# Performance work log

Measured on AMD Instinct MI355X. Metric: run time of the kernel, lower is better.

The kernel has to match this reference:

```python
import jax, jax.numpy as jnp
import numpy as np

D_MODEL = 4096
D_FF = 14336
T = 8192


def setup_inputs() -> dict:
    key = jax.random.key(0)
    k1, k2, k3, k4, k5 = jax.random.split(key, 5)
    s_in = 1.0 / np.sqrt(D_MODEL)
    s_ff = 1.0 / np.sqrt(D_FF)
    return {
        "hidden_states": jax.random.normal(k1, (T, D_MODEL), dtype=jnp.float32),
        "routing_weights": jax.random.uniform(k2, (T, 1), dtype=jnp.float32),
        "w_gate": jax.random.normal(k3, (D_MODEL, D_FF), dtype=jnp.float32) * s_in,
        "w_up": jax.random.normal(k4, (D_MODEL, D_FF), dtype=jnp.float32) * s_in,
        "w_down": jax.random.normal(k5, (D_FF, D_MODEL), dtype=jnp.float32) * s_ff,
    }


def reference(hidden_states, routing_weights, w_gate, w_up, w_down):
    # SwiGLU expert MLP: down(silu(gate(x)) * up(x)), scaled by routing weight
    gate = jnp.einsum("td,df->tf", hidden_states, w_gate)  # [T, D_FF]
    up = jnp.einsum("td,df->tf", hidden_states, w_up)      # [T, D_FF]
    h = jax.nn.silu(gate) * up                               # fused SwiGLU
    out = jnp.einsum("tf,fd->td", h, w_down)                 # [T, D_MODEL]
    return routing_weights * out
```

## Files before the change

kernel.cpp:

```cpp
#include <hip/hip_runtime.h>
#include <hip/hip_bf16.h>

using bf16 = __hip_bfloat16;
typedef __attribute__((ext_vector_type(8))) short bf16x8;
typedef __attribute__((ext_vector_type(4))) float f32x4;
typedef __attribute__((ext_vector_type(4))) int i32x4;

#define T_DIM 8192
#define DM    4096
#define DFF   14336

#define MFMA(va, vb, vc) __builtin_amdgcn_mfma_f32_16x16x32_bf16(va, vb, vc, 0, 0, 0)

__device__ __forceinline__ void gld_lds16(const bf16* gsrc, bf16* ldst) {
  auto* g = (const __attribute__((address_space(1))) unsigned int*)gsrc;
  auto* l = (__attribute__((address_space(3))) unsigned int*)ldst;
  __builtin_amdgcn_global_load_lds(g, l, 16, 0, 0);
}

__device__ __forceinline__ void stage8k(const bf16* __restrict__ gbase, long lda,
                                        long grow0, long k0, bf16* lds_tile,
                                        int gran0, int tid) {
  const int g = gran0 + tid;
  const int row = g >> 3, c16 = g & 7;
  const bf16* src = gbase + (grow0 + row) * lda + k0 + ((long)(c16 ^ (row & 7)) << 3);
  bf16* dst = lds_tile + ((size_t)(gran0 + (tid & ~63)) << 3);
  gld_lds16(src, dst);
}

#define LDA8(PB, H, M, KK) (*(const bf16x8*)(aP##KK + (PB) + (H) * 16384 + (M) * 4096))
#define LDB8(PB, N, KK)    (*(const bf16x8*)(bP##KK + (PB) + (N) * 8192))

#define PHASE_MFMA_BEGIN()                            \
  __builtin_amdgcn_s_barrier();                       \
  asm volatile("s_waitcnt lgkmcnt(0)" ::: "memory");  \
  __builtin_amdgcn_sched_barrier(0);                  \
  __builtin_amdgcn_s_setprio(1)

#define PHASE_MFMA_END()                              \
  __builtin_amdgcn_s_setprio(0);                      \
  __builtin_amdgcn_sched_barrier(0);                  \
  __builtin_amdgcn_s_barrier()

__global__ void cast_pad_kernel(const float* __restrict__ in,
                                bf16* __restrict__ out, long xlda, int n8) {
  int idx = blockIdx.x * blockDim.x + threadIdx.x;
  int stride = gridDim.x * blockDim.x;
  for (int i = idx; i < n8; i += stride) {
    const int row = i >> 9;
    const int c8 = i & 511;
    const float4 v0 = reinterpret_cast<const float4*>(in)[(long)i * 2];
    const float4 v1 = reinterpret_cast<const float4*>(in)[(long)i * 2 + 1];
    bf16 t[8] = {__float2bfloat16(v0.x), __float2bfloat16(v0.y),
                 __float2bfloat16(v0.z), __float2bfloat16(v0.w),
                 __float2bfloat16(v1.x), __float2bfloat16(v1.y),
                 __float2bfloat16(v1.z), __float2bfloat16(v1.w)};
    *reinterpret_cast<bf16x8*>(&out[(long)row * xlda + (long)c8 * 8]) =
        *reinterpret_cast<bf16x8*>(t);
  }
}

__global__ void transpose_cast_kernel(const float* __restrict__ in,
                                      bf16* __restrict__ out, int R, int C,
                                      long out_lda) {
  __shared__ float tile[32][33];
  const int c0 = blockIdx.x * 32, r0 = blockIdx.y * 32;
  const int tx = threadIdx.x, ty = threadIdx.y;
#pragma unroll
  for (int j = 0; j < 4; ++j)
    tile[ty + j * 8][tx] = in[(long)(r0 + ty + j * 8) * C + (c0 + tx)];
  __syncthreads();
#pragma unroll
  for (int j = 0; j < 4; ++j)
    out[(long)(c0 + ty + j * 8) * out_lda + (r0 + tx)] =
        __float2bfloat16(tile[tx][ty + j * 8]);
}

__global__ __launch_bounds__(512, 2) void gemm_gateup_kernel(
    const bf16* __restrict__ X, const bf16* __restrict__ Gt,
    const bf16* __restrict__ Ut, bf16* __restrict__ H,
    long ldx, long ldw, long ldh) {
  __shared__ __align__(16) bf16 smem[4 * 256 * 64 + 64 * 136];

  const int tid = threadIdx.x;
  const int lane = tid & 63, wid = tid >> 6;
  const int wm = wid >> 2, wn = wid & 3;
  const int fr = lane & 15, fg = lane >> 4;

  const int id = blockIdx.x;
  const int fsub = id & 7, bm = id >> 3;
  const long row0 = (long)bm * 256;

  bf16* const sAb = smem;
  bf16* const sBb = smem + 32768;
  bf16* const sEp = smem + 65536;

  const int inner0 = ((fg ^ (fr & 7)) << 4);
  const int inner1 = (((4 | fg) ^ (fr & 7)) << 4);
  const char* aP0 = (const char*)sAb + ((wm * 16 + fr) << 7) + inner0;
  const char* aP1 = (const char*)sAb + ((wm * 16 + fr) << 7) + inner1;
  const char* bP0 = (const char*)sBb + ((wn * 16 + fr) << 7) + inner0;
  const char* bP1 = (const char*)sBb + ((wn * 16 + fr) << 7) + inner1;

  const int r6 = tid >> 3;
  const long sc = (long)((tid & 7) ^ (r6 & 7)) << 3;
  const int tu = tid & ~63;
  const bf16* pS0 = X + (row0 + 128 + r6) * ldx + 64 + sc;
  const bf16* pS1 = X + (row0 + 192 + r6) * ldx + 64 + sc;
  const bf16* pS2 = X + (row0 +       r6) * ldx + 128 + sc;
  const bf16* pS3 = X + (row0 +  64 + r6) * ldx + 128 + sc;
  long fcol0 = (long)fsub * 128;
  const bf16* pS4 = Gt + (fcol0 +      r6) * ldw + 128 + sc;
  const bf16* pS5 = Gt + (fcol0 + 64 + r6) * ldw + 128 + sc;
  const bf16* pS6 = Ut + (fcol0 +      r6) * ldw + 128 + sc;
  const bf16* pS7 = Ut + (fcol0 + 64 + r6) * ldw + 128 + sc;
  const long BJMP = 1024 * ldw - DM;
  long fcolH = fcol0;

  f32x4 acc[8][4];
  const f32x4 z = {0.f, 0.f, 0.f, 0.f};
#pragma unroll
  for (int m = 0; m < 8; ++m)
#pragma unroll
    for (int n = 0; n < 4; ++n) acc[m][n] = z;

  stage8k(X, ldx, row0, 0, sAb, 0, tid);
  stage8k(X, ldx, row0, 0, sAb, 512, tid);
  stage8k(X, ldx, row0, 0, sAb, 1024, tid);
  stage8k(X, ldx, row0, 0, sAb, 1536, tid);
  stage8k(Gt, ldw, fcol0, 0, sBb, 0, tid);
  stage8k(Gt, ldw, fcol0, 0, sBb, 512, tid);
  stage8k(Ut, ldw, fcol0 - 128, 0, sBb, 1024, tid);
  stage8k(Ut, ldw, fcol0 - 128, 0, sBb, 1536, tid);
  stage8k(X, ldx, row0, 64, sAb + 16384, 0, tid);
  stage8k(X, ldx, row0, 64, sAb + 16384, 512, tid);
  stage8k(Gt, ldw, fcol0, 64, sBb + 16384, 0, tid);
  stage8k(Gt, ldw, fcol0, 64, sBb + 16384, 512, tid);
  stage8k(Ut, ldw, fcol0 - 128, 64, sBb + 16384, 1024, tid);
  stage8k(Ut, ldw, fcol0 - 128, 64, sBb + 16384, 1536, tid);
  asm volatile("s_waitcnt vmcnt(6)" ::: "memory");
  __builtin_amdgcn_s_barrier();

  bf16x8 a[4][2], b[4][2];
  int k1 = 64, k2 = 128;

#pragma unroll 2
  for (int g = 0; g < 896; ++g) {
    const int par = g & 1;
    const int pb = par << 15;
    bf16* aCur = sAb + par * 16384;
    bf16* bCur = sBb + par * 16384;
    bf16* aNxt = sAb + (par ^ 1) * 16384;

#pragma unroll
    for (int m = 0; m < 4; ++m) { a[m][0] = LDA8(pb, 0, m, 0); a[m][1] = LDA8(pb, 0, m, 1); }
#pragma unroll
    for (int n = 0; n < 2; ++n) { b[n][0] = LDB8(pb, n, 0); b[n][1] = LDB8(pb, n, 1); }
    gld_lds16(pS0, aNxt + ((1024 + tu) << 3));
    gld_lds16(pS1, aNxt + ((1536 + tu) << 3));
    PHASE_MFMA_BEGIN();
#pragma unroll
    for (int m = 0; m < 4; ++m)
#pragma unroll
      for (int n = 0; n < 2; ++n)
#pragma unroll
        for (int kk = 0; kk < 2; ++kk)
          acc[m][n] = MFMA(a[m][kk], b[n][kk], acc[m][n]);
    PHASE_MFMA_END();

#pragma unroll
    for (int n = 2; n < 4; ++n) { b[n][0] = LDB8(pb, n, 0); b[n][1] = LDB8(pb, n, 1); }
    gld_lds16(pS2, aCur + ((0 + tu) << 3));
    gld_lds16(pS3, aCur + ((512 + tu) << 3));
    PHASE_MFMA_BEGIN();
#pragma unroll
    for (int m = 0; m < 4; ++m)
#pragma unroll
      for (int n = 2; n < 4; ++n)
#pragma unroll
        for (int kk = 0; kk < 2; ++kk)
          acc[m][n] = MFMA(a[m][kk], b[n][kk], acc[m][n]);
    PHASE_MFMA_END();

#pragma unroll
    for (int m = 0; m < 4; ++m) { a[m][0] = LDA8(pb, 1, m, 0); a[m][1] = LDA8(pb, 1, m, 1); }
    gld_lds16(pS4, bCur + ((0 + tu) << 3));
    gld_lds16(pS5, bCur + ((512 + tu) << 3));
    PHASE_MFMA_BEGIN();
#pragma unroll
    for (int m = 0; m < 4; ++m)
#pragma unroll
      for (int n = 2; n < 4; ++n)
#pragma unroll
        for (int kk = 0; kk < 2; ++kk)
          acc[4 + m][n] = MFMA(a[m][kk], b[n][kk], acc[4 + m][n]);
    PHASE_MFMA_END();

    gld_lds16(pS6, bCur + ((1024 + tu) << 3));
    gld_lds16(pS7, bCur + ((1536 + tu) << 3));
    asm volatile("s_waitcnt vmcnt(6)" ::: "memory");
    PHASE_MFMA_BEGIN();
#pragma unroll
    for (int m = 0; m < 4; ++m)
#pragma unroll
      for (int n = 0; n < 2; ++n)
#pragma unroll
        for (int kk = 0; kk < 2; ++kk)
          acc[4 + m][n] = MFMA(a[m][kk], b[n][kk], acc[4 + m][n]);
    PHASE_MFMA_END();

    pS0 += 64; pS1 += 64;
    k1 += 64;
    if (k1 == DM) { k1 = 0; pS0 -= DM; pS1 -= DM; }
    pS2 += 64; pS3 += 64; pS4 += 64; pS5 += 64; pS6 += 64; pS7 += 64;
    k2 += 64;
    if (k2 == DM) {
      k2 = 0; pS2 -= DM; pS3 -= DM;
      pS4 += BJMP; pS5 += BJMP; pS6 += BJMP; pS7 += BJMP;
    }

    if ((g & 63) == 63) {
#pragma unroll
      for (int q = 0; q < 4; ++q) {
        __builtin_amdgcn_s_barrier();
#pragma unroll
        for (int mm = 0; mm < 2; ++mm) {
          const int m = 2 * q + mm;
          const int lr = mm * 32 + wm * 16 + fg * 4;
#pragma unroll
          for (int n = 0; n < 2; ++n) {
            const int lc = n * 64 + wn * 16 + fr;
#pragma unroll
            for (int i = 0; i < 4; ++i) {
              float gv = acc[m][n][i];
              float uv = acc[m][n + 2][i];
              float hv = (gv / (1.0f + __expf(-gv))) * uv;
              sEp[(lr + i) * 136 + lc] = __float2bfloat16(hv);
              acc[m][n][i] = 0.f;
              acc[m][n + 2][i] = 0.f;
            }
          }
        }
        asm volatile("s_waitcnt lgkmcnt(0)" ::: "memory");
        __builtin_amdgcn_s_barrier();
        {
          const int c16 = tid & 15, rb = tid >> 4;
#pragma unroll
          for (int it = 0; it < 2; ++it) {
            const int lr = rb + it * 32;
            i32x4 v = *(const i32x4*)&sEp[lr * 136 + c16 * 8];
            __builtin_nontemporal_store(
                v, (i32x4*)(H + (row0 + q * 64 + lr) * ldh + fcolH + c16 * 8));
          }
        }
      }
      fcolH += 1024;
    }
  }
}

__global__ __launch_bounds__(512, 2) void gemm_down_kernel(
    const bf16* __restrict__ A, const bf16* __restrict__ Bt,
    const float* __restrict__ routing, float* __restrict__ out,
    long ldh, long lddt) {
  __shared__ __align__(16) bf16 sA[2][256 * 64];
  __shared__ __align__(16) bf16 sB[2][256 * 64];

  const int tid = threadIdx.x;
  const int lane = tid & 63, wid = tid >> 6;
  const int wm = wid >> 2, wn = wid & 3;
  const int fr = lane & 15, fg = lane >> 4;

  const int id = blockIdx.x;
  const int xcd = id & 7, j = id >> 3;
  const int bm = j >> 1, bnl = j & 1;
  const long row0 = (long)bm * 256;
  const long col0 = (long)(xcd * 2 + bnl) * 256;
  const int NK = DFF / 64;

  const int inner0 = ((fg ^ (fr & 7)) << 4);
  const int inner1 = (((4 | fg) ^ (fr & 7)) << 4);
  const char* aP0 = (const char*)&sA[0][0] + ((wm * 16 + fr) << 7) + inner0;
  const char* aP1 = (const char*)&sA[0][0] + ((wm * 16 + fr) << 7) + inner1;
  const char* bP0 = (const char*)&sB[0][0] + ((wn * 16 + fr) << 7) + inner0;
  const char* bP1 = (const char*)&sB[0][0] + ((wn * 16 + fr) << 7) + inner1;

  const int r6 = tid >> 3;
  const long sc = (long)((tid & 7) ^ (r6 & 7)) << 3;
  const int tu = tid & ~63;
  const bf16* pS0 = A  + (row0 + 128 + r6) * ldh  + 64 + sc;
  const bf16* pS1 = A  + (row0 + 192 + r6) * ldh  + 64 + sc;
  const bf16* pS2 = A  + (row0 +       r6) * ldh  + 128 + sc;
  const bf16* pS3 = A  + (row0 +  64 + r6) * ldh  + 128 + sc;
  const bf16* pS4 = Bt + (col0 +       r6) * lddt + 128 + sc;
  const bf16* pS5 = Bt + (col0 +  64 + r6) * lddt + 128 + sc;
  const bf16* pS6 = Bt + (col0 + 128 + r6) * lddt + 128 + sc;
  const bf16* pS7 = Bt + (col0 + 192 + r6) * lddt + 128 + sc;

  f32x4 acc[8][4];
  const f32x4 z = {0.f, 0.f, 0.f, 0.f};
#pragma unroll
  for (int m = 0; m < 8; ++m)
#pragma unroll
    for (int n = 0; n < 4; ++n) acc[m][n] = z;

  stage8k(A, ldh, row0, 0, (bf16*)sA[0], 0, tid);
  stage8k(A, ldh, row0, 0, (bf16*)sA[0], 512, tid);
  stage8k(A, ldh, row0, 0, (bf16*)sA[0], 1024, tid);
  stage8k(A, ldh, row0, 0, (bf16*)sA[0], 1536, tid);
  stage8k(Bt, lddt, col0, 0, (bf16*)sB[0], 0, tid);
  stage8k(Bt, lddt, col0, 0, (bf16*)sB[0], 512, tid);
  stage8k(Bt, lddt, col0, 0, (bf16*)sB[0], 1024, tid);
  stage8k(Bt, lddt, col0, 0, (bf16*)sB[0], 1536, tid);
  stage8k(A, ldh, row0, 64, (bf16*)sA[1], 0, tid);
  stage8k(A, ldh, row0, 64, (bf16*)sA[1], 512, tid);
  stage8k(Bt, lddt, col0, 64, (bf16*)sB[1], 0, tid);
  stage8k(Bt, lddt, col0, 64, (bf16*)sB[1], 512, tid);
  stage8k(Bt, lddt, col0, 64, (bf16*)sB[1], 1024, tid);
  stage8k(Bt, lddt, col0, 64, (bf16*)sB[1], 1536, tid);
  asm volatile("s_waitcnt vmcnt(6)" ::: "memory");
  __builtin_amdgcn_s_barrier();

  bf16x8 a[4][2], b[4][2];
  int k1 = 64, k2 = 128;

#pragma unroll 2
  for (int t = 0; t < NK; ++t) {
    const int par = t & 1;
    const int pb = par << 15;
    bf16* aCur = (bf16*)sA[par];
    bf16* bCur = (bf16*)sB[par];
    bf16* aNxt = (bf16*)sA[par ^ 1];

#pragma unroll
    for (int m = 0; m < 4; ++m) { a[m][0] = LDA8(pb, 0, m, 0); a[m][1] = LDA8(pb, 0, m, 1); }
#pragma unroll
    for (int n = 0; n < 2; ++n) { b[n][0] = LDB8(pb, n, 0); b[n][1] = LDB8(pb, n, 1); }
    gld_lds16(pS0, aNxt + ((1024 + tu) << 3));
    gld_lds16(pS1, aNxt + ((1536 + tu) << 3));
    PHASE_MFMA_BEGIN();
#pragma unroll
    for (int m = 0; m < 4; ++m)
#pragma unroll
      for (int n = 0; n < 2; ++n)
#pragma unroll
        for (int kk = 0; kk < 2; ++kk)
          acc[m][n] = MFMA(a[m][kk], b[n][kk], acc[m][n]);
    PHASE_MFMA_END();

#pragma unroll
    for (int n = 2; n < 4; ++n) { b[n][0] = LDB8(pb, n, 0); b[n][1] = LDB8(pb, n, 1); }
    gld_lds16(pS2, aCur + ((0 + tu) << 3));
    gld_lds16(pS3, aCur + ((512 + tu) << 3));
    PHASE_MFMA_BEGIN();
#pragma unroll
    for (int m = 0; m < 4; ++m)
#pragma unroll
      for (int n = 2; n < 4; ++n)
#pragma unroll
        for (int kk = 0; kk < 2; ++kk)
          acc[m][n] = MFMA(a[m][kk], b[n][kk], acc[m][n]);
    PHASE_MFMA_END();

#pragma unroll
    for (int m = 0; m < 4; ++m) { a[m][0] = LDA8(pb, 1, m, 0); a[m][1] = LDA8(pb, 1, m, 1); }
    gld_lds16(pS4, bCur + ((0 + tu) << 3));
    gld_lds16(pS5, bCur + ((512 + tu) << 3));
    PHASE_MFMA_BEGIN();
#pragma unroll
    for (int m = 0; m < 4; ++m)
#pragma unroll
      for (int n = 2; n < 4; ++n)
#pragma unroll
        for (int kk = 0; kk < 2; ++kk)
          acc[4 + m][n] = MFMA(a[m][kk], b[n][kk], acc[4 + m][n]);
    PHASE_MFMA_END();

    gld_lds16(pS6, bCur + ((1024 + tu) << 3));
    gld_lds16(pS7, bCur + ((1536 + tu) << 3));
    asm volatile("s_waitcnt vmcnt(6)" ::: "memory");
    PHASE_MFMA_BEGIN();
#pragma unroll
    for (int m = 0; m < 4; ++m)
#pragma unroll
      for (int n = 0; n < 2; ++n)
#pragma unroll
        for (int kk = 0; kk < 2; ++kk)
          acc[4 + m][n] = MFMA(a[m][kk], b[n][kk], acc[4 + m][n]);
    PHASE_MFMA_END();

    pS0 += 64; pS1 += 64;
    k1 += 64;
    if (k1 == DFF) { k1 = 0; pS0 -= DFF; pS1 -= DFF; }
    pS2 += 64; pS3 += 64; pS4 += 64; pS5 += 64; pS6 += 64; pS7 += 64;
    k2 += 64;
    if (k2 == DFF) { k2 = 0; pS2 -= DFF; pS3 -= DFF; pS4 -= DFF; pS5 -= DFF; pS6 -= DFF; pS7 -= DFF; }
  }

#pragma unroll
  for (int m = 0; m < 8; ++m) {
    const long r0w = row0 + m * 32 + wm * 16 + fg * 4;
#pragma unroll
    for (int i = 0; i < 4; ++i) {
      const long r = r0w + i;
      const float rv = routing[r];
#pragma unroll
      for (int n = 0; n < 4; ++n)
        out[r * DM + (col0 + n * 64 + wn * 16 + fr)] = rv * acc[m][n][i];
    }
  }
}

extern "C" void kernel_launch(void* const* d_in, const int* in_sizes, int n_in,
                              void* d_out, int out_size, void* d_ws, size_t ws_size,
                              hipStream_t stream) {
  const float* X  = (const float*)d_in[0];
  const float* rw = (const float*)d_in[1];
  const float* Wg = (const float*)d_in[2];
  const float* Wu = (const float*)d_in[3];
  const float* Wd = (const float*)d_in[4];
  float* out = (float*)d_out;

  long XL = DM + 64, WL = DM + 64, DL = DFF + 64, HL = DFF + 64;
  {
    size_t need = 2ull * ((size_t)T_DIM * XL + 2ull * (size_t)DFF * WL +
                          (size_t)DM * DL + (size_t)T_DIM * HL);
    if (ws_size < need) { XL = DM; WL = DM; DL = DFF; HL = DFF; }
  }

  char* ws = (char*)d_ws;
  size_t off = 0;
  bf16* Xb = (bf16*)(ws + off); off += (size_t)T_DIM * XL * 2;
  bf16* GT = (bf16*)(ws + off); off += (size_t)DFF * WL * 2;
  bf16* UT = (bf16*)(ws + off); off += (size_t)DFF * WL * 2;
  bf16* DT = (bf16*)(ws + off); off += (size_t)DM * DL * 2;
  bf16* Hb = (bf16*)(ws + off); off += (size_t)T_DIM * HL * 2;

  cast_pad_kernel<<<2048, 256, 0, stream>>>(X, Xb, XL, T_DIM * DM / 8);
  dim3 tpb(32, 8);
  transpose_cast_kernel<<<dim3(DFF / 32, DM / 32), tpb, 0, stream>>>(Wg, GT, DM, DFF, WL);
  transpose_cast_kernel<<<dim3(DFF / 32, DM / 32), tpb, 0, stream>>>(Wu, UT, DM, DFF, WL);
  transpose_cast_kernel<<<dim3(DM / 32, DFF / 32), tpb, 0, stream>>>(Wd, DT, DFF, DM, DL);

  gemm_gateup_kernel<<<256, 512, 0, stream>>>(Xb, GT, UT, Hb, XL, WL, HL);
  gemm_down_kernel<<<(T_DIM / 256) * (DM / 256), 512, 0, stream>>>(
      Hb, DT, rw, out, HL, DL);
}
```

Before: 2.592 ms.

## Double-buffer LDS fragment registers to overlap LDS reads with MFMA phases

Splits the A/B register fragments into two sets and reorders the four MFMA quadrants so that the fragment loads for the next phase, and for the next k-step, are issued while the previous MFMA block runs. The explicit lgkmcnt(0) wait at each phase start is removed, leaving the compiler to insert the needed waits. The goal is to hide LDS read latency behind matrix work in both GEMM kernels. In exchange it needs more VGPRs for the fragments, and the reads of the next LDS buffer depend on its global-to-LDS loads having landed, now gated by an extra vmcnt wait placed earlier.

After: 2.683 ms. 1.03x slower.

```diff
diff --git a/kernel.cpp b/kernel.cpp
--- a/kernel.cpp
+++ b/kernel.cpp
@@ -31,15 +31,15 @@
 #define LDA8(PB, H, M, KK) (*(const bf16x8*)(aP##KK + (PB) + (H) * 16384 + (M) * 4096))
 #define LDB8(PB, N, KK)    (*(const bf16x8*)(bP##KK + (PB) + (N) * 8192))
 
-#define PHASE_MFMA_BEGIN()                            \
-  __builtin_amdgcn_s_barrier();                       \
-  asm volatile("s_waitcnt lgkmcnt(0)" ::: "memory");  \
-  __builtin_amdgcn_sched_barrier(0);                  \
+#define PH_B()                               \
+  __builtin_amdgcn_sched_barrier(0);         \
+  __builtin_amdgcn_s_barrier();              \
+  __builtin_amdgcn_sched_barrier(0);         \
   __builtin_amdgcn_s_setprio(1)
 
-#define PHASE_MFMA_END()                              \
-  __builtin_amdgcn_s_setprio(0);                      \
-  __builtin_amdgcn_sched_barrier(0);                  \
+#define PH_E()                               \
+  __builtin_amdgcn_s_setprio(0);             \
+  __builtin_amdgcn_sched_barrier(0);         \
   __builtin_amdgcn_s_barrier()
 
 __global__ void cast_pad_kernel(const float* __restrict__ in,
@@ -141,73 +141,86 @@
   asm volatile("s_waitcnt vmcnt(6)" ::: "memory");
   __builtin_amdgcn_s_barrier();
 
-  bf16x8 a[4][2], b[4][2];
+  bf16x8 a0[4][2], a1[4][2], b0[2][2], b1[2][2];
+#pragma unroll
+  for (int m = 0; m < 4; ++m) { a0[m][0] = LDA8(0, 0, m, 0); a0[m][1] = LDA8(0, 0, m, 1); }
+#pragma unroll
+  for (int n = 0; n < 2; ++n) { b0[n][0] = LDB8(0, n, 0); b0[n][1] = LDB8(0, n, 1); }
+
   int k1 = 64, k2 = 128;
 
 #pragma unroll 2
   for (int g = 0; g < 896; ++g) {
     const int par = g & 1;
     const int pb = par << 15;
+    const int nb = (par ^ 1) << 15;
     bf16* aCur = sAb + par * 16384;
     bf16* bCur = sBb + par * 16384;
     bf16* aNxt = sAb + (par ^ 1) * 16384;
 
 #pragma unroll
-    for (int m = 0; m < 4; ++m) { a[m][0] = LDA8(pb, 0, m, 0); a[m][1] = LDA8(pb, 0, m, 1); }
-#pragma unroll
-    for (int n = 0; n < 2; ++n) { b[n][0] = LDB8(pb, n, 0); b[n][1] = LDB8(pb, n, 1); }
+    for (int n = 0; n < 2; ++n) { b1[n][0] = LDB8(pb, 2 + n, 0); b1[n][1] = LDB8(pb, 2 + n, 1); }
     gld_lds16(pS0, aNxt + ((1024 + tu) << 3));
     gld_lds16(pS1, aNxt + ((1536 + tu) << 3));
-    PHASE_MFMA_BEGIN();
-#pragma unroll
-    for (int m = 0; m < 4; ++m)
-#pragma unroll
-      for (int n = 0; n < 2; ++n)
-#pragma unroll
-        for (int kk = 0; kk < 2; ++kk)
-          acc[m][n] = MFMA(a[m][kk], b[n][kk], acc[m][n]);
-    PHASE_MFMA_END();
-
-#pragma unroll
-    for (int n = 2; n < 4; ++n) { b[n][0] = LDB8(pb, n, 0); b[n][1] = LDB8(pb, n, 1); }
+    PH_B();
+#pragma unroll
+    for (int m = 0; m < 4; ++m)
+#pragma unroll
+      for (int n = 0; n < 2; ++n)
+#pragma unroll
+        for (int kk = 0; kk < 2; ++kk)
+          acc[m][n] = MFMA(a0[m][kk], b0[n][kk], acc[m][n]);
+    PH_E();
+
+#pragma unroll
+    for (int m = 0; m < 4; ++m) { a1[m][0] = LDA8(pb, 1, m, 0); a1[m][1] = LDA8(pb, 1, m, 1); }
     gld_lds16(pS2, aCur + ((0 + tu) << 3));
     gld_lds16(pS3, aCur + ((512 + tu) << 3));
-    PHASE_MFMA_BEGIN();
-#pragma unroll
-    for (int m = 0; m < 4; ++m)
-#pragma unroll
-      for (int n = 2; n < 4; ++n)
-#pragma unroll
-        for (int kk = 0; kk < 2; ++kk)
-          acc[m][n] = MFMA(a[m][kk], b[n][kk], acc[m][n]);
-    PHASE_MFMA_END();
-
-#pragma unroll
-    for (int m = 0; m < 4; ++m) { a[m][0] = LDA8(pb, 1, m, 0); a[m][1] = LDA8(pb, 1, m, 1); }
+    PH_B();
+#pragma unroll
+    for (int m = 0; m < 4; ++m)
+#pragma unroll
+      for (int n = 0; n < 2; ++n)
+#pragma unroll
+        for (int kk = 0; kk < 2; ++kk)
+          acc[m][2 + n] = MFMA(a0[m][kk], b1[n][kk], acc[m][2 + n]);
+    PH_E();
+
     gld_lds16(pS4, bCur + ((0 + tu) << 3));
     gld_lds16(pS5, bCur + ((512 + tu) << 3));
-    PHASE_MFMA_BEGIN();
-#pragma unroll
-    for (int m = 0; m < 4; ++m)
-#pragma unroll
-      for (int n = 2; n < 4; ++n)
-#pragma unroll
-        for (int kk = 0; kk < 2; ++kk)
-          acc[4 + m][n] = MFMA(a[m][kk], b[n][kk], acc[4 + m][n]);
-    PHASE_MFMA_END();
+    asm volatile("s_waitcnt vmcnt(6)" ::: "memory");
+    PH_B();
+#pragma unroll
+    for (int m = 0; m < 4; ++m)
+#pragma unroll
+      for (int n = 0; n < 2; ++n)
+#pragma unroll
+        for (int kk = 0; kk < 2; ++kk)
+          acc[4 + m][2 + n] = MFMA(a1[m][kk], b1[n][kk], acc[4 + m][2 + n]);
+    __builtin_amdgcn_s_setprio(0);
+    __builtin_amdgcn_sched_barrier(0);
+#pragma unroll
+    for (int m = 0; m < 4; ++m) { a0[m][0] = LDA8(nb, 0, m, 0); a0[m][1] = LDA8(nb, 0, m, 1); }
+    __builtin_amdgcn_sched_barrier(0);
+    __builtin_amdgcn_s_barrier();
 
     gld_lds16(pS6, bCur + ((1024 + tu) << 3));
     gld_lds16(pS7, bCur + ((1536 + tu) << 3));
     asm volatile("s_waitcnt vmcnt(6)" ::: "memory");
-    PHASE_MFMA_BEGIN();
-#pragma unroll
-    for (int m = 0; m < 4; ++m)
-#pragma unroll
-      for (int n = 0; n < 2; ++n)
-#pragma unroll
-        for (int kk = 0; kk < 2; ++kk)
-          acc[4 + m][n] = MFMA(a[m][kk], b[n][kk], acc[4 + m][n]);
-    PHASE_MFMA_END();
+    PH_B();
+#pragma unroll
+    for (int m = 0; m < 4; ++m)
+#pragma unroll
+      for (int n = 0; n < 2; ++n)
+#pragma unroll
+        for (int kk = 0; kk < 2; ++kk)
+          acc[4 + m][n] = MFMA(a1[m][kk], b0[n][kk], acc[4 + m][n]);
+    __builtin_amdgcn_s_setprio(0);
+    __builtin_amdgcn_sched_barrier(0);
+#pragma unroll
+    for (int n = 0; n < 2; ++n) { b0[n][0] = LDB8(nb, n, 0); b0[n][1] = LDB8(nb, n, 1); }
+    __builtin_amdgcn_sched_barrier(0);
+    __builtin_amdgcn_s_barrier();
 
     pS0 += 64; pS1 += 64;
     k1 += 64;
@@ -321,73 +334,86 @@
   asm volatile("s_waitcnt vmcnt(6)" ::: "memory");
   __builtin_amdgcn_s_barrier();
 
-  bf16x8 a[4][2], b[4][2];
+  bf16x8 a0[4][2], a1[4][2], b0[2][2], b1[2][2];
+#pragma unroll
+  for (int m = 0; m < 4; ++m) { a0[m][0] = LDA8(0, 0, m, 0); a0[m][1] = LDA8(0, 0, m, 1); }
+#pragma unroll
+  for (int n = 0; n < 2; ++n) { b0[n][0] = LDB8(0, n, 0); b0[n][1] = LDB8(0, n, 1); }
+
   int k1 = 64, k2 = 128;
 
 #pragma unroll 2
   for (int t = 0; t < NK; ++t) {
     const int par = t & 1;
     const int pb = par << 15;
+    const int nb = (par ^ 1) << 15;
     bf16* aCur = (bf16*)sA[par];
     bf16* bCur = (bf16*)sB[par];
     bf16* aNxt = (bf16*)sA[par ^ 1];
 
 #pragma unroll
-    for (int m = 0; m < 4; ++m) { a[m][0] = LDA8(pb, 0, m, 0); a[m][1] = LDA8(pb, 0, m, 1); }
-#pragma unroll
-    for (int n = 0; n < 2; ++n) { b[n][0] = LDB8(pb, n, 0); b[n][1] = LDB8(pb, n, 1); }
+    for (int n = 0; n < 2; ++n) { b1[n][0] = LDB8(pb, 2 + n, 0); b1[n][1] = LDB8(pb, 2 + n, 1); }
     gld_lds16(pS0, aNxt + ((1024 + tu) << 3));
     gld_lds16(pS1, aNxt + ((1536 + tu) << 3));
-    PHASE_MFMA_BEGIN();
-#pragma unroll
-    for (int m = 0; m < 4; ++m)
-#pragma unroll
-      for (int n = 0; n < 2; ++n)
-#pragma unroll
-        for (int kk = 0; kk < 2; ++kk)
-          acc[m][n] = MFMA(a[m][kk], b[n][kk], acc[m][n]);
-    PHASE_MFMA_END();
-
-#pragma unroll
-    for (int n = 2; n < 4; ++n) { b[n][0] = LDB8(pb, n, 0); b[n][1] = LDB8(pb, n, 1); }
+    PH_B();
+#pragma unroll
+    for (int m = 0; m < 4; ++m)
+#pragma unroll
+      for (int n = 0; n < 2; ++n)
+#pragma unroll
+        for (int kk = 0; kk < 2; ++kk)
+          acc[m][n] = MFMA(a0[m][kk], b0[n][kk], acc[m][n]);
+    PH_E();
+
+#pragma unroll
+    for (int m = 0; m < 4; ++m) { a1[m][0] = LDA8(pb, 1, m, 0); a1[m][1] = LDA8(pb, 1, m, 1); }
     gld_lds16(pS2, aCur + ((0 + tu) << 3));
     gld_lds16(pS3, aCur + ((512 + tu) << 3));
-    PHASE_MFMA_BEGIN();
-#pragma unroll
-    for (int m = 0; m < 4; ++m)
-#pragma unroll
-      for (int n = 2; n < 4; ++n)
-#pragma unroll
-        for (int kk = 0; kk < 2; ++kk)
-          acc[m][n] = MFMA(a[m][kk], b[n][kk], acc[m][n]);
-    PHASE_MFMA_END();
-
-#pragma unroll
-    for (int m = 0; m < 4; ++m) { a[m][0] = LDA8(pb, 1, m, 0); a[m][1] = LDA8(pb, 1, m, 1); }
+    PH_B();
+#pragma unroll
+    for (int m = 0; m < 4; ++m)
+#pragma unroll
+      for (int n = 0; n < 2; ++n)
+#pragma unroll
+        for (int kk = 0; kk < 2; ++kk)
+          acc[m][2 + n] = MFMA(a0[m][kk], b1[n][kk], acc[m][2 + n]);
+    PH_E();
+
     gld_lds16(pS4, bCur + ((0 + tu) << 3));
     gld_lds16(pS5, bCur + ((512 + tu) << 3));
-    PHASE_MFMA_BEGIN();
-#pragma unroll
-    for (int m = 0; m < 4; ++m)
-#pragma unroll
-      for (int n = 2; n < 4; ++n)
-#pragma unroll
-        for (int kk = 0; kk < 2; ++kk)
-          acc[4 + m][n] = MFMA(a[m][kk], b[n][kk], acc[4 + m][n]);
-    PHASE_MFMA_END();
+    asm volatile("s_waitcnt vmcnt(6)" ::: "memory");
+    PH_B();
+#pragma unroll
+    for (int m = 0; m < 4; ++m)
+#pragma unroll
+      for (int n = 0; n < 2; ++n)
+#pragma unroll
+        for (int kk = 0; kk < 2; ++kk)
+          acc[4 + m][2 + n] = MFMA(a1[m][kk], b1[n][kk], acc[4 + m][2 + n]);
+    __builtin_amdgcn_s_setprio(0);
+    __builtin_amdgcn_sched_barrier(0);
+#pragma unroll
+    for (int m = 0; m < 4; ++m) { a0[m][0] = LDA8(nb, 0, m, 0); a0[m][1] = LDA8(nb, 0, m, 1); }
+    __builtin_amdgcn_sched_barrier(0);
+    __builtin_amdgcn_s_barrier();
 
     gld_lds16(pS6, bCur + ((1024 + tu) << 3));
     gld_lds16(pS7, bCur + ((1536 + tu) << 3));
     asm volatile("s_waitcnt vmcnt(6)" ::: "memory");
-    PHASE_MFMA_BEGIN();
-#pragma unroll
-    for (int m = 0; m < 4; ++m)
-#pragma unroll
-      for (int n = 0; n < 2; ++n)
-#pragma unroll
-        for (int kk = 0; kk < 2; ++kk)
-          acc[4 + m][n] = MFMA(a[m][kk], b[n][kk], acc[4 + m][n]);
-    PHASE_MFMA_END();
+    PH_B();
+#pragma unroll
+    for (int m = 0; m < 4; ++m)
+#pragma unroll
+      for (int n = 0; n < 2; ++n)
+#pragma unroll
+        for (int kk = 0; kk < 2; ++kk)
+          acc[4 + m][n] = MFMA(a1[m][kk], b0[n][kk], acc[4 + m][n]);
+    __builtin_amdgcn_s_setprio(0);
+    __builtin_amdgcn_sched_barrier(0);
+#pragma unroll
+    for (int n = 0; n < 2; ++n) { b0[n][0] = LDB8(nb, n, 0); b0[n][1] = LDB8(nb, n, 1); }
+    __builtin_amdgcn_sched_barrier(0);
+    __builtin_amdgcn_s_barrier();
 
     pS0 += 64; pS1 += 64;
     k1 += 64;
```
